# Kernel tuning notes

Measured on AMD Instinct MI355X. Metric: run time of the kernel, lower is better.

## Reference

```python
import jax, jax.numpy as jnp
import numpy as np

N = 4096  # num_dev == num_task (required by elementwise msg computation)
D = 64    # embed_dim


def setup_inputs() -> dict:
    key = jax.random.key(0)
    ks = jax.random.split(key, 10)
    return {
        "embed": jax.random.normal(ks[0], (2 * N, D), jnp.float32),
        "adj_collab": jnp.zeros((N, N), jnp.float32),   # only .shape[0] is used
        "adj_interact": jnp.zeros((N, N), jnp.float32),  # unused in forward body
        "adj_similar": jnp.zeros((N, N), jnp.float32),   # unused in forward body
        "collab_score": jax.random.normal(ks[1], (N, N), jnp.float32),
        "interact_score": jax.random.normal(ks[2], (N, N), jnp.float32),
        "similar_score": jax.random.normal(ks[3], (N, N), jnp.float32),
        "deg_dev": jax.random.uniform(ks[4], (N,), jnp.float32, 1.0, 100.0),
        "deg_task": jax.random.uniform(ks[5], (N,), jnp.float32, 1.0, 100.0),
        "W1": jax.random.normal(ks[6], (D, D), jnp.float32) / np.sqrt(D).astype(np.float32),
        "b1": jnp.zeros((D,), jnp.float32),
        "W2": jax.random.normal(ks[7], (D, D), jnp.float32) / np.sqrt(D).astype(np.float32),
        "b2": jnp.zeros((D,), jnp.float32),
        "W3": jax.random.normal(ks[8], (D, D), jnp.float32) / np.sqrt(D).astype(np.float32),
        "b3": jnp.zeros((D,), jnp.float32),
    }


def _linear(x, W, b):
    # torch nn.Linear: x @ W.T + b
    return x @ W.T + b


def _calc_attention(src, dst, rel_score, src_deg, dst_deg):
    # msg = dst + src*dst ; per-row dot <src, msg> ; degree + sqrt(d) scaling ; softmax
    msg = dst + src * dst                      # [N, D]
    dot = jnp.sum(src * msg, axis=-1)          # [N]
    scale = dot / (jnp.sqrt(src_deg * dst_deg + 1e-8) * jnp.sqrt(jnp.float32(src.shape[-1])))
    att = jax.nn.softmax(rel_score * scale, axis=-1)  # [N, N] (scale broadcasts over columns)
    return att, msg


def reference(embed, adj_collab, adj_interact, adj_similar,
              collab_score, interact_score, similar_score,
              deg_dev, deg_task, W1, b1, W2, b2, W3, b3):
    num_dev = adj_collab.shape[0]
    dev = embed[:num_dev]       # [N, D]
    task = embed[num_dev:]      # [N, D]

    collab_att, collab_msg = _calc_attention(dev, dev, collab_score, deg_dev, deg_dev)
    collab_prop = collab_att @ _linear(collab_msg, W1, b1)

    interact_att, interact_msg = _calc_attention(dev, task, interact_score, deg_dev, deg_task)
    interact_prop = interact_att @ _linear(interact_msg, W2, b2)

    dev_prop = jax.nn.leaky_relu(_linear(dev + collab_prop + interact_prop, W3, b3), 0.2)

    similar_att, _similar_msg = _calc_attention(task, task, similar_score, deg_task, deg_task)
    similar_prop = similar_att @ _linear(task, W3, b3)  # note: original uses W3(task_embed), not the msg
    task_prop = jax.nn.leaky_relu(_linear(task + similar_prop, W3, b3), 0.2)

    # dropout omitted (eval mode / identity)
    return jnp.concatenate([dev_prop, task_prop], axis=0)
```

## Files before the change

### kernel.cpp

```cpp
#include <hip/hip_runtime.h>
#include <math.h>

#define N 4096
#define D 64
#define NSLICE 8
#define JLEN 512
#define CH 64
#define NCHUNK 8
#define SH 44.0f

#define S_OFF   0
#define MT_OFF  49152
#define E_OFF   65536
#define SCL_OFF 73728
#define LDS_BYTES 75776

typedef short bf16x8 __attribute__((ext_vector_type(8)));
typedef float f32x4  __attribute__((ext_vector_type(4)));

__device__ __forceinline__ unsigned short f2bf(float x) {
    unsigned int u = __float_as_uint(x);
    u += 0x7FFFu + ((u >> 16) & 1u);
    return (unsigned short)(u >> 16);
}
__device__ __forceinline__ float bf2f(unsigned short h) {
    return __uint_as_float(((unsigned int)h) << 16);
}

__device__ __forceinline__ void gld16(const void* g, void* l) {
    __builtin_amdgcn_global_load_lds(
        (const __attribute__((address_space(1))) void*)g,
        (__attribute__((address_space(3))) void*)l,
        16, 0, 0);
}

__device__ __forceinline__ void lds_barrier() {
    asm volatile("s_waitcnt lgkmcnt(0)" ::: "memory");
    __builtin_amdgcn_s_barrier();
    asm volatile("" ::: "memory");
}
__device__ __forceinline__ void plain_barrier() {
    asm volatile("" ::: "memory");
    __builtin_amdgcn_s_barrier();
    asm volatile("" ::: "memory");
}

__global__ __launch_bounds__(256) void prep_kernel(
    const float* __restrict__ embed,
    const float* __restrict__ degd, const float* __restrict__ degt,
    const float* __restrict__ W1, const float* __restrict__ b1,
    const float* __restrict__ W2, const float* __restrict__ b2,
    const float* __restrict__ W3, const float* __restrict__ b3,
    float* __restrict__ scale, unsigned short* __restrict__ Mt)
{
    const int rel = blockIdx.y;
    const float* W  = (rel == 0) ? W1 : (rel == 1 ? W2 : W3);
    const float* bb = (rel == 0) ? b1 : (rel == 1 ? b2 : b3);
    __shared__ float Wl[D][D + 1];
    __shared__ float xr[4][D];
    const int tid = threadIdx.x;
    for (int idx = tid; idx < D * D; idx += 256)
        Wl[idx >> 6][idx & 63] = W[idx];
    const int w = tid >> 6, d = tid & 63;
    const int i = blockIdx.x * 4 + w;

    float msg, term, xsrc, dga, dgb;
    if (rel == 0) {
        float s = embed[(size_t)i * D + d];
        msg = s + s * s; term = s * msg; xsrc = msg;
        dga = degd[i]; dgb = degd[i];
    } else if (rel == 1) {
        float s = embed[(size_t)i * D + d];
        float t = embed[(size_t)(N + i) * D + d];
        msg = t + s * t; term = s * msg; xsrc = msg;
        dga = degd[i]; dgb = degt[i];
    } else {
        float t = embed[(size_t)(N + i) * D + d];
        msg = t + t * t; term = t * msg; xsrc = t;
        dga = degt[i]; dgb = degt[i];
    }
    float dot = term;
    #pragma unroll
    for (int mm = 1; mm < 64; mm <<= 1) dot += __shfl_xor(dot, mm);
    if (d == 0)
        scale[rel * N + i] = dot / (sqrtf(dga * dgb + 1e-8f) * 8.0f);

    xr[w][d] = xsrc;
    __syncthreads();
    float o = bb[d];
    #pragma unroll 8
    for (int k = 0; k < D; ++k) o += xr[w][k] * Wl[d][k];
    Mt[((size_t)rel * D + d) * N + i] = f2bf(o);
}

__global__ __launch_bounds__(256, 2) void attn_kernel(
    const float* __restrict__ S0, const float* __restrict__ S1, const float* __restrict__ S2,
    const float* __restrict__ scale, const unsigned short* __restrict__ Mt,
    unsigned short* __restrict__ Up, float* __restrict__ lp)
{
    __shared__ __align__(16) char LDS[LDS_BYTES];
    const int rg = blockIdx.x, rel = blockIdx.y, sl = blockIdx.z;
    const float* S = (rel == 0) ? S0 : (rel == 1 ? S1 : S2);
    const unsigned short* Mtr = Mt + (size_t)rel * D * N;
    const int tid = threadIdx.x;
    const int lane = tid & 63, wave = tid >> 6;
    const int row = tid >> 2, q = tid & 3;
    const int j0 = sl * JLEN;

    const int sr  = wave * 4 + (lane >> 4);
    const int sgs = (lane & 15) ^ (sr & 7);
    const float* sp0 = S + (size_t)(rg * 64 +  0 + sr) * N + j0 + sgs * 4;
    const float* sp1 = S + (size_t)(rg * 64 + 16 + sr) * N + j0 + sgs * 4;
    const float* sp2 = S + (size_t)(rg * 64 + 32 + sr) * N + j0 + sgs * 4;
    const float* sp3 = S + (size_t)(rg * 64 + 48 + sr) * N + j0 + sgs * 4;
    const unsigned short* mp0 = Mtr + (size_t)lane * N + j0 + (0 * 4 + wave) * 8;
    const unsigned short* mp1 = Mtr + (size_t)lane * N + j0 + (1 * 4 + wave) * 8;

#define ISSUE_S(cc, bb) do {                                              \
        gld16(sp0 + (cc) * CH, LDS + S_OFF + (bb) * 16384 +     wave * 1024); \
        gld16(sp1 + (cc) * CH, LDS + S_OFF + (bb) * 16384 + 4096 + wave * 1024); \
        gld16(sp2 + (cc) * CH, LDS + S_OFF + (bb) * 16384 + 8192 + wave * 1024); \
        gld16(sp3 + (cc) * CH, LDS + S_OFF + (bb) * 16384 + 12288 + wave * 1024); \
    } while (0)
#define ISSUE_M(cc, bb) do {                                              \
        gld16(mp0 + (cc) * CH, LDS + MT_OFF + (bb) * 8192 + wave * 1024);       \
        gld16(mp1 + (cc) * CH, LDS + MT_OFF + (bb) * 8192 + (4 + wave) * 1024); \
    } while (0)

    for (int k = tid; k < JLEN; k += 256)
        *(float*)(LDS + SCL_OFF + k * 4) = scale[rel * N + j0 + k];
    asm volatile("" ::: "memory");
    ISSUE_M(0, 0);
    ISSUE_S(0, 0); ISSUE_S(1, 1); ISSUE_S(2, 2);
    lds_barrier();

    const int wbase = wave * 16;
    const int lrow  = lane & 15;
    const int lk    = lane >> 4;
    float l = 0.f;
    f32x4 acc[4];
    #pragma unroll
    for (int ct = 0; ct < 4; ++ct) {
        acc[ct][0] = 0.f; acc[ct][1] = 0.f; acc[ct][2] = 0.f; acc[ct][3] = 0.f;
    }

    #pragma unroll
    for (int c = 0; c < NCHUNK; ++c) {
        if (c == 0)      asm volatile("s_waitcnt vmcnt(8)" ::: "memory");
        else if (c <= 5) asm volatile("s_waitcnt vmcnt(4)" ::: "memory");
        else             asm volatile("s_waitcnt vmcnt(0)" ::: "memory");
        plain_barrier();

        if (c + 1 < NCHUNK) ISSUE_M(c + 1, (c + 1) & 1);

        {
            const char* sb = LDS + S_OFF + (c % 3) * 16384 + row * 256;
            const int r7 = row & 7;
            const f32x4 s0 = *(const f32x4*)(sb + (((q * 4 + 0) ^ r7) << 4));
            const f32x4 s1 = *(const f32x4*)(sb + (((q * 4 + 1) ^ r7) << 4));
            const f32x4 s2 = *(const f32x4*)(sb + (((q * 4 + 2) ^ r7) << 4));
            const f32x4 s3 = *(const f32x4*)(sb + (((q * 4 + 3) ^ r7) << 4));
            const char* cb = LDS + SCL_OFF + c * 256 + q * 64;
            const f32x4 c0 = *(const f32x4*)(cb);
            const f32x4 c1 = *(const f32x4*)(cb + 16);
            const f32x4 c2 = *(const f32x4*)(cb + 32);
            const f32x4 c3 = *(const f32x4*)(cb + 48);
            float e[16];
            #pragma unroll
            for (int u = 0; u < 4; ++u) {
                e[u]      = __expf(fmaf(s0[u], c0[u], -SH));
                e[4 + u]  = __expf(fmaf(s1[u], c1[u], -SH));
                e[8 + u]  = __expf(fmaf(s2[u], c2[u], -SH));
                e[12 + u] = __expf(fmaf(s3[u], c3[u], -SH));
            }
            #pragma unroll
            for (int k = 0; k < 16; ++k) l += e[k];
            union { unsigned short h[8]; uint4 v; } p0, p1;
            #pragma unroll
            for (int k = 0; k < 8; ++k) { p0.h[k] = f2bf(e[k]); p1.h[k] = f2bf(e[8 + k]); }
            const int kgA = 2 * q, kgB = 2 * q + 1;
            *(uint4*)(LDS + E_OFF + kgA * 1024 + ((row ^ kgA) << 4)) = p0.v;
            *(uint4*)(LDS + E_OFF + kgB * 1024 + ((row ^ kgB) << 4)) = p1.v;
        }

        lds_barrier();

        if (c + 3 < NCHUNK) ISSUE_S(c + 3, c % 3);

        {
            const char* mb = LDS + MT_OFF + (c & 1) * 8192;
            #pragma unroll
            for (int ks = 0; ks < 2; ++ks) {
                const int kg = ks * 4 + lk;
                const bf16x8 a = *(const bf16x8*)(
                    LDS + E_OFF + kg * 1024 + (((wbase + lrow) ^ kg) << 4));
                #pragma unroll
                for (int ct = 0; ct < 4; ++ct) {
                    const bf16x8 b = *(const bf16x8*)(mb + kg * 1024 + ((ct * 16 + lrow) << 4));
                    acc[ct] = __builtin_amdgcn_mfma_f32_16x16x32_bf16(a, b, acc[ct], 0, 0, 0);
                }
            }
        }
    }
#undef ISSUE_S
#undef ISSUE_M

    unsigned short* R = (unsigned short*)LDS;
    #pragma unroll
    for (int ct = 0; ct < 4; ++ct)
        #pragma unroll
        for (int r = 0; r < 4; ++r) {
            const int ri = wbase + lk * 4 + r;
            R[ri * 64 + ct * 16 + lrow] = f2bf(acc[ct][r]);
        }
    lds_barrier();
    const size_t pbase = (size_t)((rel * 64 + rg) * NSLICE + sl);
    unsigned short* up = Up + pbase * 4096;
    {
        const uint4* src = (const uint4*)R;
        uint4*       dst = (uint4*)up;
        dst[tid]       = src[tid];
        dst[256 + tid] = src[256 + tid];
    }
    l += __shfl_xor(l, 1);
    l += __shfl_xor(l, 2);
    if (q == 0) lp[pbase * 64 + row] = l;
}

__device__ __forceinline__ float combine_row(
    const unsigned short* __restrict__ Up, const float* __restrict__ lp,
    int rel, int i, int d)
{
    const int rg = i >> 6, r = i & 63;
    const int base = (rel * 64 + rg) * NSLICE;
    float lt = 0.f, u = 0.f;
    #pragma unroll
    for (int p = 0; p < NSLICE; ++p) {
        lt += lp[(base + p) * 64 + r];
        u  += bf2f(Up[(size_t)(base + p) * 4096 + r * 64 + d]);
    }
    return u / lt;
}

__global__ __launch_bounds__(256) void final_kernel(
    const float* __restrict__ embed,
    const unsigned short* __restrict__ Up, const float* __restrict__ lp,
    const float* __restrict__ W3, const float* __restrict__ b3,
    float* __restrict__ out)
{
    __shared__ float Wl[D][D + 1];
    __shared__ float xs[4][D];
    const int tid = threadIdx.x;
    for (int idx = tid; idx < D * D; idx += 256)
        Wl[idx >> 6][idx & 63] = W3[idx];
    const int w = tid >> 6, d = tid & 63;
    const int g = blockIdx.x * 4 + w;

    float x = embed[(size_t)g * D + d];
    if (g < N) {
        x += combine_row(Up, lp, 0, g, d);
        x += combine_row(Up, lp, 1, g, d);
    } else {
        x += combine_row(Up, lp, 2, g - N, d);
    }
    xs[w][d] = x;
    __syncthreads();
    float o = b3[d];
    #pragma unroll 8
    for (int k = 0; k < D; ++k) o += xs[w][k] * Wl[d][k];
    o = (o > 0.f) ? o : 0.2f * o;
    out[(size_t)g * D + d] = o;
}

extern "C" void kernel_launch(void* const* d_in, const int* in_sizes, int n_in,
                              void* d_out, int out_size, void* d_ws, size_t ws_size,
                              hipStream_t stream)
{
    const float* embed = (const float*)d_in[0];
    const float* Sc   = (const float*)d_in[4];
    const float* Si   = (const float*)d_in[5];
    const float* Ss   = (const float*)d_in[6];
    const float* degd = (const float*)d_in[7];
    const float* degt = (const float*)d_in[8];
    const float* W1 = (const float*)d_in[9];
    const float* b1 = (const float*)d_in[10];
    const float* W2 = (const float*)d_in[11];
    const float* b2 = (const float*)d_in[12];
    const float* W3 = (const float*)d_in[13];
    const float* b3 = (const float*)d_in[14];
    float* out = (float*)d_out;

    float* ws    = (float*)d_ws;
    float* scale = ws;
    float* lp    = ws + 12288;
    unsigned short* Mt = (unsigned short*)(lp + 98304);
    unsigned short* Up = Mt + 786432;

    prep_kernel<<<dim3(N / 4, 3), 256, 0, stream>>>(
        embed, degd, degt, W1, b1, W2, b2, W3, b3, scale, Mt);
    attn_kernel<<<dim3(64, 3, NSLICE), 256, 0, stream>>>(
        Sc, Si, Ss, scale, Mt, Up, lp);
    final_kernel<<<dim3(2 * N / 4), 256, 0, stream>>>(
        embed, Up, lp, W3, b3, out);
}
```

Before: 67.33 us.

## Replace async LDS staging with direct global loads and raise occupancy

The attention kernel no longer stages score tiles and Mt through LDS with global_load_lds and a hand-tuned triple/double buffer. Scores and scale are now read straight from global memory into registers, and MFMA B operands are loaded directly from Mt in global memory. The exp tile is double-buffered in LDS so only one barrier per chunk is needed. LDS drops to 16KB, so launch bounds rise to 4 blocks per CU to hide latency through occupancy instead of explicit prefetch. The prep kernel now gathers Mt outputs through shared memory so it writes 8-byte stores instead of scattered 2-byte stores. The trade-off is losing explicit prefetch overlap in exchange for more concurrent waves and less LDS traffic.

```diff
diff --git a/kernel.cpp b/kernel.cpp
--- a/kernel.cpp
+++ b/kernel.cpp
@@ -9,12 +9,6 @@
 #define NCHUNK 8
 #define SH 44.0f
 
-#define S_OFF   0
-#define MT_OFF  49152
-#define E_OFF   65536
-#define SCL_OFF 73728
-#define LDS_BYTES 75776
-
 typedef short bf16x8 __attribute__((ext_vector_type(8)));
 typedef float f32x4  __attribute__((ext_vector_type(4)));
 
@@ -27,20 +21,8 @@
     return __uint_as_float(((unsigned int)h) << 16);
 }
 
-__device__ __forceinline__ void gld16(const void* g, void* l) {
-    __builtin_amdgcn_global_load_lds(
-        (const __attribute__((address_space(1))) void*)g,
-        (__attribute__((address_space(3))) void*)l,
-        16, 0, 0);
-}
-
 __device__ __forceinline__ void lds_barrier() {
     asm volatile("s_waitcnt lgkmcnt(0)" ::: "memory");
-    __builtin_amdgcn_s_barrier();
-    asm volatile("" ::: "memory");
-}
-__device__ __forceinline__ void plain_barrier() {
-    asm volatile("" ::: "memory");
     __builtin_amdgcn_s_barrier();
     asm volatile("" ::: "memory");
 }
@@ -58,11 +40,13 @@
     const float* bb = (rel == 0) ? b1 : (rel == 1 ? b2 : b3);
     __shared__ float Wl[D][D + 1];
     __shared__ float xr[4][D];
+    __shared__ unsigned short ot[4][D];
     const int tid = threadIdx.x;
     for (int idx = tid; idx < D * D; idx += 256)
         Wl[idx >> 6][idx & 63] = W[idx];
     const int w = tid >> 6, d = tid & 63;
-    const int i = blockIdx.x * 4 + w;
+    const int i0 = blockIdx.x * 4;
+    const int i = i0 + w;
 
     float msg, term, xsrc, dga, dgb;
     if (rel == 0) {
@@ -90,15 +74,22 @@
     float o = bb[d];
     #pragma unroll 8
     for (int k = 0; k < D; ++k) o += xr[w][k] * Wl[d][k];
-    Mt[((size_t)rel * D + d) * N + i] = f2bf(o);
-}
-
-__global__ __launch_bounds__(256, 2) void attn_kernel(
+    ot[w][d] = f2bf(o);
+    __syncthreads();
+    if (tid < 64) {
+        union { unsigned short h[4]; uint2 v; } t;
+        t.h[0] = ot[0][tid]; t.h[1] = ot[1][tid];
+        t.h[2] = ot[2][tid]; t.h[3] = ot[3][tid];
+        *(uint2*)&Mt[((size_t)rel * D + tid) * N + i0] = t.v;
+    }
+}
+
+__global__ __launch_bounds__(256, 4) void attn_kernel(
     const float* __restrict__ S0, const float* __restrict__ S1, const float* __restrict__ S2,
     const float* __restrict__ scale, const unsigned short* __restrict__ Mt,
     unsigned short* __restrict__ Up, float* __restrict__ lp)
 {
-    __shared__ __align__(16) char LDS[LDS_BYTES];
+    __shared__ __align__(16) char EB[16384];
     const int rg = blockIdx.x, rel = blockIdx.y, sl = blockIdx.z;
     const float* S = (rel == 0) ? S0 : (rel == 1 ? S1 : S2);
     const unsigned short* Mtr = Mt + (size_t)rel * D * N;
@@ -107,36 +98,14 @@
     const int row = tid >> 2, q = tid & 3;
     const int j0 = sl * JLEN;
 
-    const int sr  = wave * 4 + (lane >> 4);
-    const int sgs = (lane & 15) ^ (sr & 7);
-    const float* sp0 = S + (size_t)(rg * 64 +  0 + sr) * N + j0 + sgs * 4;
-    const float* sp1 = S + (size_t)(rg * 64 + 16 + sr) * N + j0 + sgs * 4;
-    const float* sp2 = S + (size_t)(rg * 64 + 32 + sr) * N + j0 + sgs * 4;
-    const float* sp3 = S + (size_t)(rg * 64 + 48 + sr) * N + j0 + sgs * 4;
-    const unsigned short* mp0 = Mtr + (size_t)lane * N + j0 + (0 * 4 + wave) * 8;
-    const unsigned short* mp1 = Mtr + (size_t)lane * N + j0 + (1 * 4 + wave) * 8;
-
-#define ISSUE_S(cc, bb) do {                                              \
-        gld16(sp0 + (cc) * CH, LDS + S_OFF + (bb) * 16384 +     wave * 1024); \
-        gld16(sp1 + (cc) * CH, LDS + S_OFF + (bb) * 16384 + 4096 + wave * 1024); \
-        gld16(sp2 + (cc) * CH, LDS + S_OFF + (bb) * 16384 + 8192 + wave * 1024); \
-        gld16(sp3 + (cc) * CH, LDS + S_OFF + (bb) * 16384 + 12288 + wave * 1024); \
-    } while (0)
-#define ISSUE_M(cc, bb) do {                                              \
-        gld16(mp0 + (cc) * CH, LDS + MT_OFF + (bb) * 8192 + wave * 1024);       \
-        gld16(mp1 + (cc) * CH, LDS + MT_OFF + (bb) * 8192 + (4 + wave) * 1024); \
-    } while (0)
-
-    for (int k = tid; k < JLEN; k += 256)
-        *(float*)(LDS + SCL_OFF + k * 4) = scale[rel * N + j0 + k];
-    asm volatile("" ::: "memory");
-    ISSUE_M(0, 0);
-    ISSUE_S(0, 0); ISSUE_S(1, 1); ISSUE_S(2, 2);
-    lds_barrier();
+    const float* Sp   = S + (size_t)(rg * 64 + row) * N + j0 + q * 16;
+    const float* sclp = scale + rel * N + j0 + q * 16;
 
     const int wbase = wave * 16;
     const int lrow  = lane & 15;
     const int lk    = lane >> 4;
+    const unsigned short* bbp = Mtr + (size_t)lrow * N + j0 + lk * 8;
+
     float l = 0.f;
     f32x4 acc[4];
     #pragma unroll
@@ -144,27 +113,23 @@
         acc[ct][0] = 0.f; acc[ct][1] = 0.f; acc[ct][2] = 0.f; acc[ct][3] = 0.f;
     }
 
+    const int kgA = 2 * q, kgB = 2 * q + 1;
+    char* ewA = EB + kgA * 1024 + ((row ^ kgA) << 4);
+    char* ewB = EB + kgB * 1024 + ((row ^ kgB) << 4);
+
     #pragma unroll
     for (int c = 0; c < NCHUNK; ++c) {
-        if (c == 0)      asm volatile("s_waitcnt vmcnt(8)" ::: "memory");
-        else if (c <= 5) asm volatile("s_waitcnt vmcnt(4)" ::: "memory");
-        else             asm volatile("s_waitcnt vmcnt(0)" ::: "memory");
-        plain_barrier();
-
-        if (c + 1 < NCHUNK) ISSUE_M(c + 1, (c + 1) & 1);
+        const int cb = (c & 1) * 8192;
 
         {
-            const char* sb = LDS + S_OFF + (c % 3) * 16384 + row * 256;
-            const int r7 = row & 7;
-            const f32x4 s0 = *(const f32x4*)(sb + (((q * 4 + 0) ^ r7) << 4));
-            const f32x4 s1 = *(const f32x4*)(sb + (((q * 4 + 1) ^ r7) << 4));
-            const f32x4 s2 = *(const f32x4*)(sb + (((q * 4 + 2) ^ r7) << 4));
-            const f32x4 s3 = *(const f32x4*)(sb + (((q * 4 + 3) ^ r7) << 4));
-            const char* cb = LDS + SCL_OFF + c * 256 + q * 64;
-            const f32x4 c0 = *(const f32x4*)(cb);
-            const f32x4 c1 = *(const f32x4*)(cb + 16);
-            const f32x4 c2 = *(const f32x4*)(cb + 32);
-            const f32x4 c3 = *(const f32x4*)(cb + 48);
+            const f32x4 s0 = *(const f32x4*)(Sp + c * CH + 0);
+            const f32x4 s1 = *(const f32x4*)(Sp + c * CH + 4);
+            const f32x4 s2 = *(const f32x4*)(Sp + c * CH + 8);
+            const f32x4 s3 = *(const f32x4*)(Sp + c * CH + 12);
+            const f32x4 c0 = *(const f32x4*)(sclp + c * CH + 0);
+            const f32x4 c1 = *(const f32x4*)(sclp + c * CH + 4);
+            const f32x4 c2 = *(const f32x4*)(sclp + c * CH + 8);
+            const f32x4 c3 = *(const f32x4*)(sclp + c * CH + 12);
             float e[16];
             #pragma unroll
             for (int u = 0; u < 4; ++u) {
@@ -178,34 +143,26 @@
             union { unsigned short h[8]; uint4 v; } p0, p1;
             #pragma unroll
             for (int k = 0; k < 8; ++k) { p0.h[k] = f2bf(e[k]); p1.h[k] = f2bf(e[8 + k]); }
-            const int kgA = 2 * q, kgB = 2 * q + 1;
-            *(uint4*)(LDS + E_OFF + kgA * 1024 + ((row ^ kgA) << 4)) = p0.v;
-            *(uint4*)(LDS + E_OFF + kgB * 1024 + ((row ^ kgB) << 4)) = p1.v;
+            *(uint4*)(ewA + cb) = p0.v;
+            *(uint4*)(ewB + cb) = p1.v;
         }
 
         lds_barrier();
 
-        if (c + 3 < NCHUNK) ISSUE_S(c + 3, c % 3);
-
-        {
-            const char* mb = LDS + MT_OFF + (c & 1) * 8192;
-            #pragma unroll
-            for (int ks = 0; ks < 2; ++ks) {
-                const int kg = ks * 4 + lk;
-                const bf16x8 a = *(const bf16x8*)(
-                    LDS + E_OFF + kg * 1024 + (((wbase + lrow) ^ kg) << 4));
-                #pragma unroll
-                for (int ct = 0; ct < 4; ++ct) {
-                    const bf16x8 b = *(const bf16x8*)(mb + kg * 1024 + ((ct * 16 + lrow) << 4));
-                    acc[ct] = __builtin_amdgcn_mfma_f32_16x16x32_bf16(a, b, acc[ct], 0, 0, 0);
-                }
+        #pragma unroll
+        for (int ks = 0; ks < 2; ++ks) {
+            const int kg = ks * 4 + lk;
+            const bf16x8 a = *(const bf16x8*)(
+                EB + cb + kg * 1024 + (((wbase + lrow) ^ kg) << 4));
+            #pragma unroll
+            for (int ct = 0; ct < 4; ++ct) {
+                const bf16x8 b = *(const bf16x8*)(bbp + (size_t)ct * 16 * N + c * CH + ks * 32);
+                acc[ct] = __builtin_amdgcn_mfma_f32_16x16x32_bf16(a, b, acc[ct], 0, 0, 0);
             }
         }
     }
-#undef ISSUE_S
-#undef ISSUE_M
-
-    unsigned short* R = (unsigned short*)LDS;
+
+    unsigned short* R = (unsigned short*)EB;
     #pragma unroll
     for (int ct = 0; ct < 4; ++ct)
         #pragma unroll
```

Measured after the change: 91.74 us. +36.3%, slower.
